# Optimization experiments

Measured on AMD Instinct MI355X. Metric: run time of the kernel, lower is better.

The kernel has to match this reference:

```python
import jax, jax.numpy as jnp
import numpy as np


def setup_inputs() -> dict:
    key = jax.random.key(0)
    ks = jax.random.split(key, 8)
    B, C, D, H, W = 4, 128, 16, 16, 16
    Cqk = C // 8  # out_channels // 8 = 16
    return {
        "x": jax.random.normal(ks[0], (B, C, D, H, W), dtype=jnp.float32),
        "Wq": jax.random.normal(ks[1], (Cqk, C), dtype=jnp.float32) * 0.05,
        "bq": jax.random.normal(ks[2], (Cqk,), dtype=jnp.float32) * 0.05,
        "Wk": jax.random.normal(ks[3], (Cqk, C), dtype=jnp.float32) * 0.05,
        "bk": jax.random.normal(ks[4], (Cqk,), dtype=jnp.float32) * 0.05,
        "Wv": jax.random.normal(ks[5], (C, C), dtype=jnp.float32) * 0.05,
        "bv": jax.random.normal(ks[6], (C,), dtype=jnp.float32) * 0.05,
        "gamma": jax.random.normal(ks[7], (1,), dtype=jnp.float32),
    }


def reference(x, Wq, bq, Wk, bk, Wv, bv, gamma):
    B, C, D, H, W = x.shape
    xf = x.reshape(B, C, D * H * W)  # b c n
    # 1x1x1 Conv3d == channel-wise GEMM
    q = jnp.einsum('oc,bcn->bon', Wq, xf) + bq[None, :, None]  # [B, Cqk, N]
    k = jnp.einsum('oc,bcn->bon', Wk, xf) + bk[None, :, None]  # [B, Cqk, N]
    v = jnp.einsum('oc,bcn->bon', Wv, xf) + bv[None, :, None]  # [B, C,   N]
    # attention[b, n, m] = sum_c q[b,c,n] * k[b,c,m]  (NO 1/sqrt(d) scaling, faithful)
    attn = jax.nn.softmax(jnp.einsum('bcn,bcm->bnm', q, k), axis=-1)  # [B, N, N]
    out = jnp.einsum('bcm,bnm->bcn', v, attn)  # [B, C, N]
    out = out.reshape(B, C, D, H, W)
    return gamma * out + x
```

## Files before the change

kernel.cpp:

```cpp
#include <hip/hip_runtime.h>


typedef __attribute__((ext_vector_type(8))) short short8;
typedef __attribute__((ext_vector_type(4))) float f32x4;

#define NTOK 4096
#define CDIM 128

__device__ __forceinline__ unsigned short f2bf(float f) {
  unsigned int u = __float_as_uint(f);
  return (unsigned short)((u + 0x7fffu + ((u >> 16) & 1u)) >> 16);
}

__global__ __launch_bounds__(256) void sa3d_proj(
    const float* __restrict__ x,
    const float* __restrict__ Wq, const float* __restrict__ bq,
    const float* __restrict__ Wk, const float* __restrict__ bk,
    const float* __restrict__ Wv, const float* __restrict__ bv,
    unsigned short* __restrict__ qb, unsigned short* __restrict__ kb,
    unsigned short* __restrict__ vb)
{
  __shared__ unsigned short Wl[160 * 136];
  __shared__ unsigned short xT[64 * 136];
  const int tid = threadIdx.x;
  const int b = (blockIdx.x & 7) >> 1;
  const int nt = ((blockIdx.x >> 3) << 1) | (blockIdx.x & 1);
  const int n0 = nt << 6;

  for (int i = 0; i < 80; ++i) {
    int idx = i * 256 + tid;
    int o = idx >> 7, c = idx & 127;
    float wv;
    if (o < 16)      wv = Wq[o * 128 + c];
    else if (o < 32) wv = Wk[(o - 16) * 128 + c];
    else             wv = Wv[(o - 32) * 128 + c];
    Wl[o * 136 + c] = f2bf(wv);
  }
  {
    int nn = tid & 63, cg = tid >> 6;
    const float* xp = x + (size_t)b * CDIM * NTOK + n0 + nn;
    for (int cp = 0; cp < 16; ++cp) {
      int c = cg * 32 + cp * 2;
      float v0 = xp[(size_t)c * NTOK];
      float v1 = xp[(size_t)(c + 1) * NTOK];
      *(unsigned int*)&xT[nn * 136 + c] =
          (unsigned int)f2bf(v0) | ((unsigned int)f2bf(v1) << 16);
    }
  }
  __syncthreads();

  const int w = tid >> 6, lane = tid & 63;
  const int l15 = lane & 15, g = lane >> 4;

  short8 bfr[4];
#pragma unroll
  for (int ks = 0; ks < 4; ++ks)
    bfr[ks] = *(const short8*)&xT[(w * 16 + l15) * 136 + ks * 32 + g * 8];

  const int n = n0 + w * 16 + l15;
#pragma unroll
  for (int ot = 0; ot < 10; ++ot) {
    f32x4 acc = {};
#pragma unroll
    for (int ks = 0; ks < 4; ++ks) {
      short8 af = *(const short8*)&Wl[(ot * 16 + l15) * 136 + ks * 32 + g * 8];
      acc = __builtin_amdgcn_mfma_f32_16x16x32_bf16(af, bfr[ks], acc, 0, 0, 0);
    }
    int ob = ot * 16 + 4 * g;
    if (ot == 0) {
      unsigned int p0 = (unsigned int)f2bf(acc[0] + bq[ob]) |
                        ((unsigned int)f2bf(acc[1] + bq[ob + 1]) << 16);
      unsigned int p1 = (unsigned int)f2bf(acc[2] + bq[ob + 2]) |
                        ((unsigned int)f2bf(acc[3] + bq[ob + 3]) << 16);
      unsigned int* d = (unsigned int*)&qb[((size_t)b * NTOK + n) * 16 + ob];
      d[0] = p0; d[1] = p1;
    } else if (ot == 1) {
      int o2 = ob - 16;
      unsigned int p0 = (unsigned int)f2bf(acc[0] + bk[o2]) |
                        ((unsigned int)f2bf(acc[1] + bk[o2 + 1]) << 16);
      unsigned int p1 = (unsigned int)f2bf(acc[2] + bk[o2 + 2]) |
                        ((unsigned int)f2bf(acc[3] + bk[o2 + 3]) << 16);
      unsigned int* d = (unsigned int*)&kb[((size_t)b * NTOK + n) * 16 + o2];
      d[0] = p0; d[1] = p1;
    } else {
#pragma unroll
      for (int r = 0; r < 4; ++r) {
        int o = ob + r - 32;
        size_t eidx = (size_t)(o >> 4) * 65536 + (size_t)(n >> 5) * 512 +
                      (size_t)((n >> 3) & 3) * 128 + (o & 15) * 8 + (n & 7);
        vb[(size_t)b * (CDIM * NTOK) + eidx] = f2bf(acc[r] + bv[o]);
      }
    }
  }
}

__global__ __launch_bounds__(512, 2) void sa3d_attn(
    const unsigned short* __restrict__ qb, const unsigned short* __restrict__ kb,
    const unsigned short* __restrict__ vb,
    const float* __restrict__ x, const float* __restrict__ gamma,
    float* __restrict__ out)
{
  __shared__ __align__(16) unsigned char smem[66560];

  const int tid = threadIdx.x;
  const int w = tid >> 6, lane = tid & 63;
  const int l15 = lane & 15, g = lane >> 4;
  const int b = (blockIdx.x & 7) >> 1;
  const int qt = ((blockIdx.x >> 3) << 1) | (blockIdx.x & 1);
  const int q0 = qt << 5;

  unsigned short* PLw = (unsigned short*)smem + w * 2304;
  float* LDp = (float*)(smem + 65536);

  const unsigned short* qbase = qb + (size_t)b * NTOK * 16;
  const unsigned short* kbase = kb + (size_t)b * NTOK * 16;
  const unsigned short* vbase = vb + (size_t)b * CDIM * NTOK;

  short8 aq[2] = {short8{}, short8{}};
#pragma unroll
  for (int qh = 0; qh < 2; ++qh)
    if (g < 2)
      aq[qh] = *(const short8*)&qbase[(size_t)(q0 + qh * 16 + l15) * 16 + g * 8];

  f32x4 acc[16];
#pragma unroll
  for (int i = 0; i < 16; ++i) acc[i] = (f32x4){};
  float Lp[2][4] = {{0.f, 0.f, 0.f, 0.f}, {0.f, 0.f, 0.f, 0.f}};

  const int kv0 = w << 9;

  short8 kfa[4], kfb[4];
#pragma unroll
  for (int kt = 0; kt < 4; ++kt) {
    kfa[kt] = short8{};
    if (g < 2)
      kfa[kt] = *(const short8*)&kbase[(size_t)(kv0 + kt * 16 + l15) * 16 + g * 8];
  }

#define SA_ITER(T, KC, KN)                                                    \
  {                                                                           \
    const int m0 = kv0 + ((T) << 6);                                          \
    const int mb5 = m0 >> 5;                                                  \
    short8 vf[16];                                                            \
    _Pragma("unroll") for (int ch = 0; ch < 2; ++ch)                          \
      _Pragma("unroll") for (int ct = 0; ct < 8; ++ct)                        \
        vf[ch * 8 + ct] = *(const short8*)&vbase[(size_t)ct * 65536 +         \
                                                 (size_t)(mb5 + ch) * 512 +   \
                                                 g * 128 + l15 * 8];          \
    _Pragma("unroll") for (int kt = 0; kt < 4; ++kt) {                        \
      _Pragma("unroll") for (int qh = 0; qh < 2; ++qh) {                      \
        f32x4 zero = {};                                                      \
        f32x4 s = __builtin_amdgcn_mfma_f32_16x16x32_bf16(aq[qh], KC[kt],     \
                                                          zero, 0, 0, 0);     \
        _Pragma("unroll") for (int r = 0; r < 4; ++r) {                       \
          float e = __expf(s[r]);                                             \
          Lp[qh][r] += e;                                                     \
          PLw[(qh * 16 + 4 * g + r) * 72 + kt * 16 + l15] = f2bf(e);          \
        }                                                                     \
      }                                                                       \
    }                                                                         \
    const int mn = kv0 + (((T) + 1 < 8 ? (T) + 1 : 0) << 6);                  \
    _Pragma("unroll") for (int kt = 0; kt < 4; ++kt) {                        \
      KN[kt] = short8{};                                                      \
      if (g < 2)                                                              \
        KN[kt] = *(const short8*)&kbase[(size_t)(mn + kt * 16 + l15) * 16 +   \
                                        g * 8];                               \
    }                                                                         \
    _Pragma("unroll") for (int ch = 0; ch < 2; ++ch) {                        \
      short8 pa0 = *(const short8*)&PLw[l15 * 72 + ch * 32 + g * 8];          \
      short8 pa1 = *(const short8*)&PLw[(16 + l15) * 72 + ch * 32 + g * 8];   \
      _Pragma("unroll") for (int ct = 0; ct < 8; ++ct) {                      \
        acc[ct] = __builtin_amdgcn_mfma_f32_16x16x32_bf16(pa0, vf[ch * 8 + ct], \
                                                          acc[ct], 0, 0, 0); \
        acc[8 + ct] = __builtin_amdgcn_mfma_f32_16x16x32_bf16(                \
            pa1, vf[ch * 8 + ct], acc[8 + ct], 0, 0, 0);                      \
      }                                                                       \
    }                                                                         \
  }

  for (int tt = 0; tt < 4; ++tt) {
    SA_ITER(tt * 2, kfa, kfb);
    SA_ITER(tt * 2 + 1, kfb, kfa);
  }
#undef SA_ITER

#pragma unroll
  for (int qh = 0; qh < 2; ++qh)
#pragma unroll
    for (int r = 0; r < 4; ++r) {
      float v = Lp[qh][r];
      v += __shfl_xor(v, 1);
      v += __shfl_xor(v, 2);
      v += __shfl_xor(v, 4);
      v += __shfl_xor(v, 8);
      Lp[qh][r] = v;
    }

  const int rowb = lane * 256;
  const int sw = (l15) << 4;

#define ACC_STORE(i)                                                        \
  {                                                                         \
    char* base = (char*)smem + (i) * 16384 + rowb;                          \
    _Pragma("unroll") for (int j = 0; j < 16; ++j)                          \
        *(f32x4*)(base + ((j * 16) ^ sw)) = acc[j];                         \
    if (l15 == 0) {                                                         \
      _Pragma("unroll") for (int qh = 0; qh < 2; ++qh)                      \
          _Pragma("unroll") for (int r = 0; r < 4; ++r)                     \
              LDp[(i) * 32 + qh * 16 + 4 * g + r] = Lp[qh][r];              \
    }                                                                       \
  }
#define ACC_ADD(i)                                                          \
  {                                                                         \
    char* base = (char*)smem + (i) * 16384 + rowb;                          \
    _Pragma("unroll") for (int j = 0; j < 16; ++j)                          \
        acc[j] += *(const f32x4*)(base + ((j * 16) ^ sw));                  \
    _Pragma("unroll") for (int qh = 0; qh < 2; ++qh)                        \
        _Pragma("unroll") for (int r = 0; r < 4; ++r)                       \
            Lp[qh][r] += LDp[(i) * 32 + qh * 16 + 4 * g + r];               \
  }

  __syncthreads();
  if (w >= 4) ACC_STORE(w - 4);
  __syncthreads();
  if (w < 4) ACC_ADD(w);
  __syncthreads();
  if (w == 2 || w == 3) ACC_STORE(w - 2);
  __syncthreads();
  if (w < 2) ACC_ADD(w);
  __syncthreads();
  if (w == 1) ACC_STORE(0);
  __syncthreads();

  if (w == 0) {
    ACC_ADD(0);
    const float ga = gamma[0];
    float inv[2][4];
#pragma unroll
    for (int qh = 0; qh < 2; ++qh)
#pragma unroll
      for (int r = 0; r < 4; ++r) inv[qh][r] = 1.0f / Lp[qh][r];

    const float* xb = x + (size_t)b * CDIM * NTOK;
    float* ob = out + (size_t)b * CDIM * NTOK;
#pragma unroll
    for (int qh = 0; qh < 2; ++qh)
#pragma unroll
      for (int ct = 0; ct < 8; ++ct) {
        int c = ct * 16 + l15;
        size_t idx = (size_t)c * NTOK + q0 + qh * 16 + 4 * g;
        f32x4 xv = *(const f32x4*)&xb[idx];
        f32x4 o;
#pragma unroll
        for (int r = 0; r < 4; ++r)
          o[r] = ga * acc[qh * 8 + ct][r] * inv[qh][r] + xv[r];
        *(f32x4*)&ob[idx] = o;
      }
  }
}

extern "C" void kernel_launch(void* const* d_in, const int* in_sizes, int n_in,
                              void* d_out, int out_size, void* d_ws, size_t ws_size,
                              hipStream_t stream) {
  const float* x     = (const float*)d_in[0];
  const float* Wq    = (const float*)d_in[1];
  const float* bq    = (const float*)d_in[2];
  const float* Wk    = (const float*)d_in[3];
  const float* bk    = (const float*)d_in[4];
  const float* Wv    = (const float*)d_in[5];
  const float* bv    = (const float*)d_in[6];
  const float* gamma = (const float*)d_in[7];

  unsigned short* qb = (unsigned short*)d_ws;
  unsigned short* kb = qb + (size_t)4 * NTOK * 16;
  unsigned short* vb = kb + (size_t)4 * NTOK * 16;
  float* outp = (float*)d_out;

  sa3d_proj<<<dim3(256), dim3(256), 0, stream>>>(x, Wq, bq, Wk, bk, Wv, bv,
                                                 qb, kb, vb);
  sa3d_attn<<<dim3(512), dim3(512), 0, stream>>>(qb, kb, vb, x, gamma, outp);
}
```

Before: 56.78 us.

## Split attention block across key and channel groups with shared double-buffered P

Restructures the attention kernel so each block handles 16 queries, with waves split into two key halves and four channel groups. The groups share a double-buffered probability tile in LDS and synchronize every iteration. Shared memory and registers are greatly reduced to allow many more resident blocks, and the grid is doubled. The trade-off is a block barrier per key tile, smaller per-wave MFMA work, and a more frequent cross-wave reduction.

```diff
diff --git a/kernel.cpp b/kernel.cpp
--- a/kernel.cpp
+++ b/kernel.cpp
@@ -94,168 +94,166 @@
   }
 }
 
-__global__ __launch_bounds__(512, 2) void sa3d_attn(
+__global__ __launch_bounds__(512, 8) void sa3d_attn(
     const unsigned short* __restrict__ qb, const unsigned short* __restrict__ kb,
     const unsigned short* __restrict__ vb,
     const float* __restrict__ x, const float* __restrict__ gamma,
     float* __restrict__ out)
 {
-  __shared__ __align__(16) unsigned char smem[66560];
+  __shared__ __align__(16) unsigned char smem[9728];
+  unsigned short* P = (unsigned short*)smem;
+  float* LDp = (float*)(smem + 9216);
 
   const int tid = threadIdx.x;
   const int w = tid >> 6, lane = tid & 63;
   const int l15 = lane & 15, g = lane >> 4;
+  const int kg = w >> 2, cg = w & 3;
   const int b = (blockIdx.x & 7) >> 1;
   const int qt = ((blockIdx.x >> 3) << 1) | (blockIdx.x & 1);
-  const int q0 = qt << 5;
-
-  unsigned short* PLw = (unsigned short*)smem + w * 2304;
-  float* LDp = (float*)(smem + 65536);
+  const int q0 = qt << 4;
 
   const unsigned short* qbase = qb + (size_t)b * NTOK * 16;
   const unsigned short* kbase = kb + (size_t)b * NTOK * 16;
   const unsigned short* vbase = vb + (size_t)b * CDIM * NTOK;
 
-  short8 aq[2] = {short8{}, short8{}};
-#pragma unroll
-  for (int qh = 0; qh < 2; ++qh)
+  short8 aq = short8{};
+  if (g < 2) aq = *(const short8*)&qbase[(size_t)(q0 + l15) * 16 + g * 8];
+
+  f32x4 acc[2];
+  acc[0] = (f32x4){}; acc[1] = (f32x4){};
+  float Lp[4] = {0.f, 0.f, 0.f, 0.f};
+
+  const int kv0 = kg << 11;
+  const int kcol = (cg << 4) + l15;
+  const int pkg = kg * 1152;
+
+  {
+    short8 kf = short8{};
     if (g < 2)
-      aq[qh] = *(const short8*)&qbase[(size_t)(q0 + qh * 16 + l15) * 16 + g * 8];
-
-  f32x4 acc[16];
-#pragma unroll
-  for (int i = 0; i < 16; ++i) acc[i] = (f32x4){};
-  float Lp[2][4] = {{0.f, 0.f, 0.f, 0.f}, {0.f, 0.f, 0.f, 0.f}};
-
-  const int kv0 = w << 9;
-
-  short8 kfa[4], kfb[4];
-#pragma unroll
-  for (int kt = 0; kt < 4; ++kt) {
-    kfa[kt] = short8{};
+      kf = *(const short8*)&kbase[(size_t)(kv0 + kcol) * 16 + g * 8];
+    f32x4 z = {};
+    f32x4 s = __builtin_amdgcn_mfma_f32_16x16x32_bf16(aq, kf, z, 0, 0, 0);
+#pragma unroll
+    for (int r = 0; r < 4; ++r) {
+      float e = __expf(s[r]);
+      Lp[r] += e;
+      P[pkg + (4 * g + r) * 72 + kcol] = f2bf(e);
+    }
+  }
+  __syncthreads();
+
+#pragma unroll 2
+  for (int t = 0; t < 31; ++t) {
+    const int bufc = t & 1, bufp = bufc ^ 1;
+    const int mrow = (kv0 >> 5) + t * 2;
+    short8 vf[4];
+#pragma unroll
+    for (int ct2 = 0; ct2 < 2; ++ct2)
+#pragma unroll
+      for (int ch = 0; ch < 2; ++ch)
+        vf[ct2 * 2 + ch] = *(const short8*)&vbase[
+            (size_t)(cg * 2 + ct2) * 65536 + (size_t)(mrow + ch) * 512 +
+            g * 128 + l15 * 8];
+    short8 kf = short8{};
     if (g < 2)
-      kfa[kt] = *(const short8*)&kbase[(size_t)(kv0 + kt * 16 + l15) * 16 + g * 8];
-  }
-
-#define SA_ITER(T, KC, KN)                                                    \
-  {                                                                           \
-    const int m0 = kv0 + ((T) << 6);                                          \
-    const int mb5 = m0 >> 5;                                                  \
-    short8 vf[16];                                                            \
-    _Pragma("unroll") for (int ch = 0; ch < 2; ++ch)                          \
-      _Pragma("unroll") for (int ct = 0; ct < 8; ++ct)                        \
-        vf[ch * 8 + ct] = *(const short8*)&vbase[(size_t)ct * 65536 +         \
-                                                 (size_t)(mb5 + ch) * 512 +   \
-                                                 g * 128 + l15 * 8];          \
-    _Pragma("unroll") for (int kt = 0; kt < 4; ++kt) {                        \
-      _Pragma("unroll") for (int qh = 0; qh < 2; ++qh) {                      \
-        f32x4 zero = {};                                                      \
-        f32x4 s = __builtin_amdgcn_mfma_f32_16x16x32_bf16(aq[qh], KC[kt],     \
-                                                          zero, 0, 0, 0);     \
-        _Pragma("unroll") for (int r = 0; r < 4; ++r) {                       \
-          float e = __expf(s[r]);                                             \
-          Lp[qh][r] += e;                                                     \
-          PLw[(qh * 16 + 4 * g + r) * 72 + kt * 16 + l15] = f2bf(e);          \
-        }                                                                     \
-      }                                                                       \
-    }                                                                         \
-    const int mn = kv0 + (((T) + 1 < 8 ? (T) + 1 : 0) << 6);                  \
-    _Pragma("unroll") for (int kt = 0; kt < 4; ++kt) {                        \
-      KN[kt] = short8{};                                                      \
-      if (g < 2)                                                              \
-        KN[kt] = *(const short8*)&kbase[(size_t)(mn + kt * 16 + l15) * 16 +   \
-                                        g * 8];                               \
-    }                                                                         \
-    _Pragma("unroll") for (int ch = 0; ch < 2; ++ch) {                        \
-      short8 pa0 = *(const short8*)&PLw[l15 * 72 + ch * 32 + g * 8];          \
-      short8 pa1 = *(const short8*)&PLw[(16 + l15) * 72 + ch * 32 + g * 8];   \
-      _Pragma("unroll") for (int ct = 0; ct < 8; ++ct) {                      \
-        acc[ct] = __builtin_amdgcn_mfma_f32_16x16x32_bf16(pa0, vf[ch * 8 + ct], \
-                                                          acc[ct], 0, 0, 0); \
-        acc[8 + ct] = __builtin_amdgcn_mfma_f32_16x16x32_bf16(                \
-            pa1, vf[ch * 8 + ct], acc[8 + ct], 0, 0, 0);                      \
-      }                                                                       \
-    }                                                                         \
-  }
-
-  for (int tt = 0; tt < 4; ++tt) {
-    SA_ITER(tt * 2, kfa, kfb);
-    SA_ITER(tt * 2 + 1, kfb, kfa);
-  }
-#undef SA_ITER
-
-#pragma unroll
-  for (int qh = 0; qh < 2; ++qh)
-#pragma unroll
-    for (int r = 0; r < 4; ++r) {
-      float v = Lp[qh][r];
-      v += __shfl_xor(v, 1);
-      v += __shfl_xor(v, 2);
-      v += __shfl_xor(v, 4);
-      v += __shfl_xor(v, 8);
-      Lp[qh][r] = v;
-    }
-
-  const int rowb = lane * 256;
-  const int sw = (l15) << 4;
-
-#define ACC_STORE(i)                                                        \
-  {                                                                         \
-    char* base = (char*)smem + (i) * 16384 + rowb;                          \
-    _Pragma("unroll") for (int j = 0; j < 16; ++j)                          \
-        *(f32x4*)(base + ((j * 16) ^ sw)) = acc[j];                         \
-    if (l15 == 0) {                                                         \
-      _Pragma("unroll") for (int qh = 0; qh < 2; ++qh)                      \
-          _Pragma("unroll") for (int r = 0; r < 4; ++r)                     \
-              LDp[(i) * 32 + qh * 16 + 4 * g + r] = Lp[qh][r];              \
-    }                                                                       \
-  }
-#define ACC_ADD(i)                                                          \
-  {                                                                         \
-    char* base = (char*)smem + (i) * 16384 + rowb;                          \
-    _Pragma("unroll") for (int j = 0; j < 16; ++j)                          \
-        acc[j] += *(const f32x4*)(base + ((j * 16) ^ sw));                  \
-    _Pragma("unroll") for (int qh = 0; qh < 2; ++qh)                        \
-        _Pragma("unroll") for (int r = 0; r < 4; ++r)                       \
-            Lp[qh][r] += LDp[(i) * 32 + qh * 16 + 4 * g + r];               \
-  }
-
-  __syncthreads();
-  if (w >= 4) ACC_STORE(w - 4);
-  __syncthreads();
-  if (w < 4) ACC_ADD(w);
-  __syncthreads();
-  if (w == 2 || w == 3) ACC_STORE(w - 2);
-  __syncthreads();
-  if (w < 2) ACC_ADD(w);
-  __syncthreads();
-  if (w == 1) ACC_STORE(0);
-  __syncthreads();
-
-  if (w == 0) {
-    ACC_ADD(0);
+      kf = *(const short8*)&kbase[
+          (size_t)(kv0 + ((t + 1) << 6) + kcol) * 16 + g * 8];
+    short8 pa[2];
+#pragma unroll
+    for (int ch = 0; ch < 2; ++ch)
+      pa[ch] = *(const short8*)&P[bufc * 2304 + pkg + l15 * 72 + ch * 32 + g * 8];
+    {
+      f32x4 z = {};
+      f32x4 s = __builtin_amdgcn_mfma_f32_16x16x32_bf16(aq, kf, z, 0, 0, 0);
+#pragma unroll
+      for (int r = 0; r < 4; ++r) {
+        float e = __expf(s[r]);
+        Lp[r] += e;
+        P[bufp * 2304 + pkg + (4 * g + r) * 72 + kcol] = f2bf(e);
+      }
+    }
+    __builtin_amdgcn_s_setprio(1);
+#pragma unroll
+    for (int ct2 = 0; ct2 < 2; ++ct2)
+#pragma unroll
+      for (int ch = 0; ch < 2; ++ch)
+        acc[ct2] = __builtin_amdgcn_mfma_f32_16x16x32_bf16(
+            pa[ch], vf[ct2 * 2 + ch], acc[ct2], 0, 0, 0);
+    __builtin_amdgcn_s_setprio(0);
+    __syncthreads();
+  }
+  {
+    const int mrow = (kv0 >> 5) + 62;
+    short8 vf[4];
+#pragma unroll
+    for (int ct2 = 0; ct2 < 2; ++ct2)
+#pragma unroll
+      for (int ch = 0; ch < 2; ++ch)
+        vf[ct2 * 2 + ch] = *(const short8*)&vbase[
+            (size_t)(cg * 2 + ct2) * 65536 + (size_t)(mrow + ch) * 512 +
+            g * 128 + l15 * 8];
+    short8 pa[2];
+#pragma unroll
+    for (int ch = 0; ch < 2; ++ch)
+      pa[ch] = *(const short8*)&P[2304 + pkg + l15 * 72 + ch * 32 + g * 8];
+    __builtin_amdgcn_s_setprio(1);
+#pragma unroll
+    for (int ct2 = 0; ct2 < 2; ++ct2)
+#pragma unroll
+      for (int ch = 0; ch < 2; ++ch)
+        acc[ct2] = __builtin_amdgcn_mfma_f32_16x16x32_bf16(
+            pa[ch], vf[ct2 * 2 + ch], acc[ct2], 0, 0, 0);
+    __builtin_amdgcn_s_setprio(0);
+  }
+
+#pragma unroll
+  for (int r = 0; r < 4; ++r) {
+    float v = Lp[r];
+    v += __shfl_xor(v, 1);
+    v += __shfl_xor(v, 2);
+    v += __shfl_xor(v, 4);
+    v += __shfl_xor(v, 8);
+    Lp[r] = v;
+  }
+  if (l15 == 0) {
+    f32x4 lv;
+    lv[0] = Lp[0]; lv[1] = Lp[1]; lv[2] = Lp[2]; lv[3] = Lp[3];
+    *(f32x4*)&LDp[w * 16 + 4 * g] = lv;
+  }
+  __syncthreads();
+
+  float* RED = (float*)smem;
+  if (kg == 1) {
+    *(f32x4*)&RED[cg * 512 + lane * 4] = acc[0];
+    *(f32x4*)&RED[cg * 512 + 256 + lane * 4] = acc[1];
+  }
+  __syncthreads();
+
+  if (kg == 0) {
+    acc[0] += *(const f32x4*)&RED[cg * 512 + lane * 4];
+    acc[1] += *(const f32x4*)&RED[cg * 512 + 256 + lane * 4];
+    f32x4 Lt = {};
+#pragma unroll
+    for (int w8 = 0; w8 < 8; ++w8)
+      Lt += *(const f32x4*)&LDp[w8 * 16 + 4 * g];
     const float ga = gamma[0];
-    float inv[2][4];
-#pragma unroll
-    for (int qh = 0; qh < 2; ++qh)
-#pragma unroll
-      for (int r = 0; r < 4; ++r) inv[qh][r] = 1.0f / Lp[qh][r];
+    f32x4 inv;
+#pragma unroll
+    for (int r = 0; r < 4; ++r) inv[r] = 1.0f / Lt[r];
 
     const float* xb = x + (size_t)b * CDIM * NTOK;
     float* ob = out + (size_t)b * CDIM * NTOK;
 #pragma unroll
-    for (int qh = 0; qh < 2; ++qh)
-#pragma unroll
-      for (int ct = 0; ct < 8; ++ct) {
-        int c = ct * 16 + l15;
-        size_t idx = (size_t)c * NTOK + q0 + qh * 16 + 4 * g;
-        f32x4 xv = *(const f32x4*)&xb[idx];
-        f32x4 o;
-#pragma unroll
-        for (int r = 0; r < 4; ++r)
-          o[r] = ga * acc[qh * 8 + ct][r] * inv[qh][r] + xv[r];
-        *(f32x4*)&ob[idx] = o;
-      }
+    for (int ct2 = 0; ct2 < 2; ++ct2) {
+      int c = cg * 32 + ct2 * 16 + l15;
+      size_t idx = (size_t)c * NTOK + q0 + 4 * g;
+      f32x4 xv = *(const f32x4*)&xb[idx];
+      f32x4 o;
+#pragma unroll
+      for (int r = 0; r < 4; ++r)
+        o[r] = ga * acc[ct2][r] * inv[r] + xv[r];
+      *(f32x4*)&ob[idx] = o;
+    }
   }
 }
 
@@ -278,5 +276,5 @@
 
   sa3d_proj<<<dim3(256), dim3(256), 0, stream>>>(x, Wq, bq, Wk, bk, Wv, bv,
                                                  qb, kb, vb);
-  sa3d_attn<<<dim3(512), dim3(512), 0, stream>>>(qb, kb, vb, x, gamma, outp);
-}
+  sa3d_attn<<<dim3(1024), dim3(512), 0, stream>>>(qb, kb, vb, x, gamma, outp);
+}
```

Measured after the change: 173.9 us. +206.3%, slower.

## Software-pipeline softmax exp and PV MFMA with double-buffered P tiles

Applied to the files above, without the earlier changes.

Restructures the attention loop so the QK^T plus exp step for tile T+1 is issued while the PV MFMAs for tile T run, using two P buffers per wave in LDS. Folds log2(e) into Wq and bq so the kernel can call exp2 directly, and packs bf16 conversion with v_cvt_pk_bf16_f32. Changes the V layout so each 64-token tile is contiguous, and raises MFMA priority with s_setprio. The cost is a larger LDS footprint and more register pressure, which could reduce occupancy.

```diff
diff --git a/kernel.cpp b/kernel.cpp
--- a/kernel.cpp
+++ b/kernel.cpp
@@ -6,6 +6,7 @@
 
 #define NTOK 4096
 #define CDIM 128
+#define L2E 1.44269504088896340736f
 
 __device__ __forceinline__ unsigned short f2bf(float f) {
   unsigned int u = __float_as_uint(f);
@@ -31,7 +32,7 @@
     int idx = i * 256 + tid;
     int o = idx >> 7, c = idx & 127;
     float wv;
-    if (o < 16)      wv = Wq[o * 128 + c];
+    if (o < 16)      wv = Wq[o * 128 + c] * L2E;
     else if (o < 32) wv = Wk[(o - 16) * 128 + c];
     else             wv = Wv[(o - 32) * 128 + c];
     Wl[o * 136 + c] = f2bf(wv);
@@ -68,10 +69,10 @@
     }
     int ob = ot * 16 + 4 * g;
     if (ot == 0) {
-      unsigned int p0 = (unsigned int)f2bf(acc[0] + bq[ob]) |
-                        ((unsigned int)f2bf(acc[1] + bq[ob + 1]) << 16);
-      unsigned int p1 = (unsigned int)f2bf(acc[2] + bq[ob + 2]) |
-                        ((unsigned int)f2bf(acc[3] + bq[ob + 3]) << 16);
+      unsigned int p0 = (unsigned int)f2bf(acc[0] + bq[ob] * L2E) |
+                        ((unsigned int)f2bf(acc[1] + bq[ob + 1] * L2E) << 16);
+      unsigned int p1 = (unsigned int)f2bf(acc[2] + bq[ob + 2] * L2E) |
+                        ((unsigned int)f2bf(acc[3] + bq[ob + 3] * L2E) << 16);
       unsigned int* d = (unsigned int*)&qb[((size_t)b * NTOK + n) * 16 + ob];
       d[0] = p0; d[1] = p1;
     } else if (ot == 1) {
@@ -86,7 +87,8 @@
 #pragma unroll
       for (int r = 0; r < 4; ++r) {
         int o = ob + r - 32;
-        size_t eidx = (size_t)(o >> 4) * 65536 + (size_t)(n >> 5) * 512 +
+        size_t eidx = (size_t)(n >> 6) * 8192 +
+                      (size_t)((o >> 4) * 2 + ((n >> 5) & 1)) * 512 +
                       (size_t)((n >> 3) & 3) * 128 + (o & 15) * 8 + (n & 7);
         vb[(size_t)b * (CDIM * NTOK) + eidx] = f2bf(acc[r] + bv[o]);
       }
@@ -100,7 +102,7 @@
     const float* __restrict__ x, const float* __restrict__ gamma,
     float* __restrict__ out)
 {
-  __shared__ __align__(16) unsigned char smem[66560];
+  __shared__ __align__(16) unsigned char smem[73728];
 
   const int tid = threadIdx.x;
   const int w = tid >> 6, lane = tid & 63;
@@ -109,7 +111,7 @@
   const int qt = ((blockIdx.x >> 3) << 1) | (blockIdx.x & 1);
   const int q0 = qt << 5;
 
-  unsigned short* PLw = (unsigned short*)smem + w * 2304;
+  unsigned short* PLw = (unsigned short*)(smem + w * 9216);
   float* LDp = (float*)(smem + 65536);
 
   const unsigned short* qbase = qb + (size_t)b * NTOK * 16;
@@ -128,61 +130,119 @@
   float Lp[2][4] = {{0.f, 0.f, 0.f, 0.f}, {0.f, 0.f, 0.f, 0.f}};
 
   const int kv0 = w << 9;
+  const int voff = g * 128 + l15 * 8;
+  const unsigned short* vtile = vbase + (size_t)(kv0 >> 6) * 8192;
 
   short8 kfa[4], kfb[4];
 #pragma unroll
   for (int kt = 0; kt < 4; ++kt) {
     kfa[kt] = short8{};
-    if (g < 2)
+    kfb[kt] = short8{};
+    if (g < 2) {
       kfa[kt] = *(const short8*)&kbase[(size_t)(kv0 + kt * 16 + l15) * 16 + g * 8];
-  }
-
-#define SA_ITER(T, KC, KN)                                                    \
+      kfb[kt] = *(const short8*)&kbase[(size_t)(kv0 + 64 + kt * 16 + l15) * 16 + g * 8];
+    }
+  }
+
+#define SA_PRODUCE(TN, KC)                                                    \
   {                                                                           \
-    const int m0 = kv0 + ((T) << 6);                                          \
-    const int mb5 = m0 >> 5;                                                  \
-    short8 vf[16];                                                            \
-    _Pragma("unroll") for (int ch = 0; ch < 2; ++ch)                          \
-      _Pragma("unroll") for (int ct = 0; ct < 8; ++ct)                        \
-        vf[ch * 8 + ct] = *(const short8*)&vbase[(size_t)ct * 65536 +         \
-                                                 (size_t)(mb5 + ch) * 512 +   \
-                                                 g * 128 + l15 * 8];          \
+    const int pbn = ((TN) & 1) * 2304;                                        \
     _Pragma("unroll") for (int kt = 0; kt < 4; ++kt) {                        \
       _Pragma("unroll") for (int qh = 0; qh < 2; ++qh) {                      \
-        f32x4 zero = {};                                                      \
+        f32x4 z = {};                                                         \
         f32x4 s = __builtin_amdgcn_mfma_f32_16x16x32_bf16(aq[qh], KC[kt],     \
-                                                          zero, 0, 0, 0);     \
-        _Pragma("unroll") for (int r = 0; r < 4; ++r) {                       \
-          float e = __expf(s[r]);                                             \
-          Lp[qh][r] += e;                                                     \
-          PLw[(qh * 16 + 4 * g + r) * 72 + kt * 16 + l15] = f2bf(e);          \
-        }                                                                     \
+                                                          z, 0, 0, 0);        \
+        float e0 = __builtin_exp2f(s[0]);                                     \
+        float e1 = __builtin_exp2f(s[1]);                                     \
+        float e2 = __builtin_exp2f(s[2]);                                     \
+        float e3 = __builtin_exp2f(s[3]);                                     \
+        Lp[qh][0] += e0; Lp[qh][1] += e1;                                     \
+        Lp[qh][2] += e2; Lp[qh][3] += e3;                                     \
+        unsigned int pk0, pk1;                                                \
+        asm("v_cvt_pk_bf16_f32 %0, %1, %2" : "=v"(pk0) : "v"(e0), "v"(e1));   \
+        asm("v_cvt_pk_bf16_f32 %0, %1, %2" : "=v"(pk1) : "v"(e2), "v"(e3));   \
+        const int rb = pbn + (qh * 16 + 4 * g) * 72 + kt * 16 + l15;          \
+        PLw[rb]       = (unsigned short)pk0;                                  \
+        PLw[rb + 72]  = (unsigned short)(pk0 >> 16);                          \
+        PLw[rb + 144] = (unsigned short)pk1;                                  \
+        PLw[rb + 216] = (unsigned short)(pk1 >> 16);                          \
       }                                                                       \
     }                                                                         \
-    const int mn = kv0 + (((T) + 1 < 8 ? (T) + 1 : 0) << 6);                  \
-    _Pragma("unroll") for (int kt = 0; kt < 4; ++kt) {                        \
-      KN[kt] = short8{};                                                      \
-      if (g < 2)                                                              \
-        KN[kt] = *(const short8*)&kbase[(size_t)(mn + kt * 16 + l15) * 16 +   \
-                                        g * 8];                               \
+  }
+
+#define SA_ITER(T, KC, KN, PREF)                                              \
+  {                                                                           \
+    const int pbo = ((T) & 1) * 2304;                                         \
+    short8 pa[2][2];                                                          \
+    _Pragma("unroll") for (int qh = 0; qh < 2; ++qh)                          \
+      _Pragma("unroll") for (int ch = 0; ch < 2; ++ch)                        \
+        pa[qh][ch] = *(const short8*)&PLw[pbo + (qh * 16 + l15) * 72 +        \
+                                          ch * 32 + g * 8];                   \
+    short8 vf[16];                                                            \
+    {                                                                         \
+      const unsigned short* vt = vtile + (size_t)(T) * 8192;                  \
+      _Pragma("unroll") for (int ct = 0; ct < 8; ++ct)                        \
+        _Pragma("unroll") for (int ch = 0; ch < 2; ++ch)                      \
+          vf[ch * 8 + ct] = *(const short8*)&vt[(ct * 2 + ch) * 512 + voff];  \
     }                                                                         \
-    _Pragma("unroll") for (int ch = 0; ch < 2; ++ch) {                        \
-      short8 pa0 = *(const short8*)&PLw[l15 * 72 + ch * 32 + g * 8];          \
-      short8 pa1 = *(const short8*)&PLw[(16 + l15) * 72 + ch * 32 + g * 8];   \
-      _Pragma("unroll") for (int ct = 0; ct < 8; ++ct) {                      \
-        acc[ct] = __builtin_amdgcn_mfma_f32_16x16x32_bf16(pa0, vf[ch * 8 + ct], \
-                                                          acc[ct], 0, 0, 0); \
-        acc[8 + ct] = __builtin_amdgcn_mfma_f32_16x16x32_bf16(                \
-            pa1, vf[ch * 8 + ct], acc[8 + ct], 0, 0, 0);                      \
+    SA_PRODUCE((T) + 1, KC);                                                  \
+    if (PREF) {                                                               \
+      _Pragma("unroll") for (int kt = 0; kt < 4; ++kt) {                      \
+        KN[kt] = short8{};                                                    \
+        if (g < 2)                                                            \
+          KN[kt] = *(const short8*)&kbase[                                    \
+              (size_t)(kv0 + (((T) + 2) << 6) + kt * 16 + l15) * 16 + g * 8]; \
       }                                                                       \
     }                                                                         \
-  }
-
-  for (int tt = 0; tt < 4; ++tt) {
-    SA_ITER(tt * 2, kfa, kfb);
-    SA_ITER(tt * 2 + 1, kfb, kfa);
-  }
+    __builtin_amdgcn_s_setprio(1);                                            \
+    _Pragma("unroll") for (int ch = 0; ch < 2; ++ch)                          \
+      _Pragma("unroll") for (int ct = 0; ct < 8; ++ct) {                      \
+        acc[ct] = __builtin_amdgcn_mfma_f32_16x16x32_bf16(                    \
+            pa[0][ch], vf[ch * 8 + ct], acc[ct], 0, 0, 0);                    \
+        acc[8 + ct] = __builtin_amdgcn_mfma_f32_16x16x32_bf16(                \
+            pa[1][ch], vf[ch * 8 + ct], acc[8 + ct], 0, 0, 0);                \
+      }                                                                       \
+    __builtin_amdgcn_s_setprio(0);                                            \
+  }
+
+#define SA_TAIL(T)                                                            \
+  {                                                                           \
+    const int pbo = ((T) & 1) * 2304;                                         \
+    short8 pa[2][2];                                                          \
+    _Pragma("unroll") for (int qh = 0; qh < 2; ++qh)                          \
+      _Pragma("unroll") for (int ch = 0; ch < 2; ++ch)                        \
+        pa[qh][ch] = *(const short8*)&PLw[pbo + (qh * 16 + l15) * 72 +        \
+                                          ch * 32 + g * 8];                   \
+    short8 vf[16];                                                            \
+    {                                                                         \
+      const unsigned short* vt = vtile + (size_t)(T) * 8192;                  \
+      _Pragma("unroll") for (int ct = 0; ct < 8; ++ct)                        \
+        _Pragma("unroll") for (int ch = 0; ch < 2; ++ch)                      \
+          vf[ch * 8 + ct] = *(const short8*)&vt[(ct * 2 + ch) * 512 + voff];  \
+    }                                                                         \
+    __builtin_amdgcn_s_setprio(1);                                            \
+    _Pragma("unroll") for (int ch = 0; ch < 2; ++ch)                          \
+      _Pragma("unroll") for (int ct = 0; ct < 8; ++ct) {                      \
+        acc[ct] = __builtin_amdgcn_mfma_f32_16x16x32_bf16(                    \
+            pa[0][ch], vf[ch * 8 + ct], acc[ct], 0, 0, 0);                    \
+        acc[8 + ct] = __builtin_amdgcn_mfma_f32_16x16x32_bf16(                \
+            pa[1][ch], vf[ch * 8 + ct], acc[8 + ct], 0, 0, 0);                \
+      }                                                                       \
+    __builtin_amdgcn_s_setprio(0);                                            \
+  }
+
+  SA_PRODUCE(0, kfa);
+  SA_ITER(0, kfb, kfa, 1);
+  SA_ITER(1, kfa, kfb, 1);
+  SA_ITER(2, kfb, kfa, 1);
+  SA_ITER(3, kfa, kfb, 1);
+  SA_ITER(4, kfb, kfa, 1);
+  SA_ITER(5, kfa, kfb, 1);
+  SA_ITER(6, kfb, kfa, 0);
+  SA_TAIL(7);
+#undef SA_PRODUCE
 #undef SA_ITER
+#undef SA_TAIL
 
 #pragma unroll
   for (int qh = 0; qh < 2; ++qh)
```

New measurement: 147.3 us. 2.59x slower.
